# Kernel tuning notes

Hardware: AMD Instinct MI355X
Metric: run time of the kernel (lower is better)

## Reference

```python
import jax, jax.numpy as jnp
import numpy as np

POOL = 2

def conv1x1(x, w, b):
    # x: [B,C,H,W], w: [O,C], b: [O]
    return jnp.einsum('bchw,oc->bohw', x, w) + b[None, :, None, None]

def setup_inputs() -> dict:
    key = jax.random.key(0)
    ks = jax.random.split(key, 8)
    B, C, H, W = 4, 256, 128, 128
    C8 = C // 8
    x = jax.random.normal(ks[0], (B, C, H, W), dtype=jnp.float32)
    wq = jax.random.normal(ks[1], (C8, C), dtype=jnp.float32) * 0.05
    bq = jax.random.normal(ks[2], (C8,), dtype=jnp.float32) * 0.01
    wk = jax.random.normal(ks[3], (C8, C), dtype=jnp.float32) * 0.05
    bk = jax.random.normal(ks[4], (C8,), dtype=jnp.float32) * 0.01
    wv = jax.random.normal(ks[5], (C, C), dtype=jnp.float32) * 0.05
    bv = jax.random.normal(ks[6], (C,), dtype=jnp.float32) * 0.01
    gamma = jnp.full((1,), 0.5, dtype=jnp.float32)  # module inits to 0; nonzero for a meaningful baseline
    return {"x": x, "wq": wq, "bq": bq, "wk": wk, "bk": bk, "wv": wv, "bv": bv, "gamma": gamma}

def reference(x, wq, bq, wk, bk, wv, bv, gamma):
    B, C, H, W = x.shape
    y = x
    # AvgPool2d(pool_size=2)
    Hp, Wp = H // POOL, W // POOL
    xp = x.reshape(B, C, Hp, POOL, Wp, POOL).mean(axis=(3, 5))
    N = Hp * Wp
    q = conv1x1(xp, wq, bq).reshape(B, -1, N)            # [B, C/8, N]
    k = conv1x1(xp, wk, bk).reshape(B, -1, N)            # [B, C/8, N]
    v = conv1x1(xp, wv, bv).reshape(B, C, N)             # [B, C, N]
    energy = jnp.einsum('bcn,bcm->bnm', q, k)            # [B, N, N]
    attn = jax.nn.softmax(energy, axis=-1)
    out = jnp.einsum('bcm,bnm->bcn', v, attn)            # [B, C, N]
    out = out.reshape(B, C, Hp, Wp)
    # bilinear upsample x2, align_corners=False == half-pixel == jax.image.resize 'linear'
    up = jax.image.resize(out, (B, C, H, W), method='bilinear')
    return gamma[0] * up + y
```

## Files before the change

kernel.cpp:

```cpp
#include <hip/hip_runtime.h>

#define BB 4
#define CC 256
#define HH 128
#define WW 128
#define HP 64
#define NP 4096

#define L2E 1.4426950408889634f

typedef __attribute__((ext_vector_type(4)))  float f32x4;
typedef __attribute__((ext_vector_type(16))) float f32x16;
typedef __attribute__((ext_vector_type(8)))  short bf16x8;
typedef __attribute__((ext_vector_type(4)))  unsigned int u32x4;
typedef __attribute__((ext_vector_type(2)))  unsigned int u32x2;
typedef __attribute__((ext_vector_type(2)))  __bf16 bf16x2_t;

static __device__ __forceinline__ float exp2fast(float x) {
    return __builtin_amdgcn_exp2f(x);
}

static __device__ __forceinline__ unsigned short f2bf(float f) {
    unsigned int u = __float_as_uint(f);
    u = (u + 0x7FFFu + ((u >> 16) & 1u)) >> 16;
    return (unsigned short)u;
}
static __device__ __forceinline__ unsigned int pk2(float a, float b) {
    bf16x2_t v = {(__bf16)a, (__bf16)b};
    return __builtin_bit_cast(unsigned int, v);
}
static __device__ __forceinline__ u32x2 plswap(unsigned int a, unsigned int b) {
    return __builtin_amdgcn_permlane32_swap(a, b, false, false);
}


__global__ __launch_bounds__(256) void prep_kernel(const float* __restrict__ x,
                                                   const float* __restrict__ wq,
                                                   const float* __restrict__ wk,
                                                   const float* __restrict__ wv,
                                                   unsigned short* __restrict__ xfrag,
                                                   unsigned short* __restrict__ wfrag) {
    if (blockIdx.x < 2048) {
        int tid  = blockIdx.x * 256 + threadIdx.x;
        int lane = tid & 63;
        int ks   = (tid >> 6) & 15;
        int nt   = (tid >> 10) & 127;
        int b    = tid >> 17;

        int n  = nt * 32 + (lane & 31);
        int c0 = ks * 16 + (lane >> 5) * 8;
        int hp = n >> 6, wp = n & 63;

        const float* xb = x + (size_t)b * CC * (HH * WW) + (2 * hp) * WW + 2 * wp;
        unsigned short r[8];
        #pragma unroll
        for (int e = 0; e < 8; e++) {
            const float* src = xb + (size_t)(c0 + e) * (HH * WW);
            float2 a = *(const float2*)(src);
            float2 d = *(const float2*)(src + WW);
            r[e] = f2bf(0.25f * (a.x + a.y + d.x + d.y));
        }
        ushort4 lo = (ushort4){r[0], r[1], r[2], r[3]};
        ushort4 hi = (ushort4){r[4], r[5], r[6], r[7]};
        *(ushort4*)(xfrag + (size_t)tid * 8)     = lo;
        *(ushort4*)(xfrag + (size_t)tid * 8 + 4) = hi;
    } else {
        int tid  = (blockIdx.x - 2048) * 256 + threadIdx.x;
        if (tid >= 10240) return;
        int lane = tid & 63;
        int ks   = (tid >> 6) & 15;
        int ot   = tid >> 10;

        int o = ot * 32 + (lane & 31);
        int c = ks * 16 + (lane >> 5) * 8;
        const float* wrow;
        float scale = 1.0f;
        if (o < 32)      { wrow = wq + (size_t)o * CC;        scale = L2E; }
        else if (o < 64) { wrow = wk + (size_t)(o - 32) * CC; }
        else             { wrow = wv + (size_t)(o - 64) * CC; }
        float4 w0 = *(const float4*)(wrow + c);
        float4 w1 = *(const float4*)(wrow + c + 4);
        ushort4 lo = {f2bf(w0.x * scale), f2bf(w0.y * scale), f2bf(w0.z * scale), f2bf(w0.w * scale)};
        ushort4 hi = {f2bf(w1.x * scale), f2bf(w1.y * scale), f2bf(w1.z * scale), f2bf(w1.w * scale)};
        *(ushort4*)(wfrag + (size_t)tid * 8)     = lo;
        *(ushort4*)(wfrag + (size_t)tid * 8 + 4) = hi;
    }
}

__global__ __launch_bounds__(128) void projm_kernel(const unsigned short* __restrict__ xfrag,
                                                    const unsigned short* __restrict__ wfrag,
                                                    const float* __restrict__ bq,
                                                    const float* __restrict__ bk,
                                                    const float* __restrict__ bv,
                                                    unsigned short* __restrict__ qarr,
                                                    unsigned short* __restrict__ karr,
                                                    unsigned short* __restrict__ varr) {
    int j    = blockIdx.x;
    int og   = j % 5;
    int nt   = (j / 5) & 127;
    int b    = j / 640;
    int lane = threadIdx.x & 63;
    int ot   = og * 2 + (threadIdx.x >> 6);

    const unsigned short* abase = wfrag + ((size_t)ot * 16 * 64 + lane) * 8;
    const unsigned short* bbase = xfrag + (((size_t)(b * 128 + nt) * 16) * 64 + lane) * 8;

    f32x16 acc;
    #pragma unroll
    for (int r = 0; r < 16; r++) acc[r] = 0.f;

    #pragma unroll
    for (int ks = 0; ks < 16; ks++) {
        bf16x8 af = *(const bf16x8*)(abase + (size_t)ks * 512);
        bf16x8 bf = *(const bf16x8*)(bbase + (size_t)ks * 512);
        acc = __builtin_amdgcn_mfma_f32_32x32x16_bf16(af, bf, acc, 0, 0, 0);
    }

    int l31 = lane & 31;
    int hi2 = lane >> 5;

    if (ot == 0) {
        unsigned short* qb = qarr + (size_t)b * (NP * 32);
        #pragma unroll
        for (int r = 0; r < 16; r++) {
            int o = (r & 3) + 8 * (r >> 2) + 4 * hi2;
            float v = acc[r] + bq[o] * L2E;
            size_t idx = (((size_t)nt * 2 + (o >> 4)) * 32 + l31) * 16 + ((o >> 3) & 1) * 8 + (o & 7);
            qb[idx] = f2bf(v);
        }
    } else if (ot == 1) {
        unsigned short* kb = karr + (size_t)b * (NP * 32);
        #pragma unroll
        for (int r = 0; r < 16; r++) {
            int o = (r & 3) + 8 * (r >> 2) + 4 * hi2;
            float v = acc[r] + bk[o];
            size_t idx = (((size_t)nt * 2 + (o >> 4)) * 32 + l31) * 16 + ((o >> 3) & 1) * 8 + (o & 7);
            kb[idx] = f2bf(v);
        }
    } else {
        unsigned short* vb = varr + (size_t)b * (CC * NP);
        int kc = nt, w2 = (l31 >> 4) & 1, hiv = (l31 >> 3) & 1, ev = l31 & 7;
        size_t base = (((size_t)kc * 2 + w2) * 8) * 32 * 16 + hiv * 8 + ev;
        #pragma unroll
        for (int r = 0; r < 16; r++) {
            int c = (ot - 2) * 32 + (r & 3) + 8 * (r >> 2) + 4 * hi2;
            float v = acc[r] + bv[c];
            size_t idx = base + ((size_t)(c >> 5) * 32 + (c & 31)) * 16;
            vb[idx] = f2bf(v);
        }
    }
}

__global__ __launch_bounds__(256, 2) void flash32_kernel(const unsigned short* __restrict__ qarr,
                                                         const unsigned short* __restrict__ karr,
                                                         const unsigned short* __restrict__ varr,
                                                         float* __restrict__ att) {
    __shared__ float cacc[64][140];
    __shared__ float cml[64][2];
    int t    = threadIdx.x;
    int lane = t & 63;
    int ks   = t >> 6;
    int j    = blockIdx.x;
    int b    = j & 3;
    int qt   = j >> 2;

    const unsigned short* qb2 = qarr + (size_t)b * (NP * 32);
    const unsigned short* kb2 = karr + (size_t)b * (NP * 32);
    const unsigned short* vb2 = varr + (size_t)b * (CC * NP);

    int q  = lane & 31;
    int hi = lane >> 5;
    int lq16 = (q * 2 + hi) * 8;

    bf16x8 qf0 = *(const bf16x8*)(qb2 + (size_t)(qt * 2 + 0) * 512 + lq16);
    bf16x8 qf1 = *(const bf16x8*)(qb2 + (size_t)(qt * 2 + 1) * 512 + lq16);

    f32x16 acc[8];
    #pragma unroll
    for (int ct = 0; ct < 8; ct++)
        #pragma unroll
        for (int r = 0; r < 16; r++) acc[ct][r] = 0.f;
    float mrun = -3.0e38f, lrun = 0.f;

    const f32x16 z16 = {0.f,0.f,0.f,0.f,0.f,0.f,0.f,0.f,0.f,0.f,0.f,0.f,0.f,0.f,0.f,0.f};

    int kc0 = ks * 32;
    const unsigned short* kcp0 = kb2 + (size_t)kc0 * 1024 + lq16;
    bf16x8 kcur0 = *(const bf16x8*)(kcp0);
    bf16x8 kcur1 = *(const bf16x8*)(kcp0 + 512);
    bf16x8 vfA[8], vfB[8];
    {
        const unsigned short* vcp0 = vb2 + ((size_t)kc0 * 16) * 512 + lq16;
        #pragma unroll
        for (int i = 0; i < 8; i++) vfA[i] = *(const bf16x8*)(vcp0 + (size_t)i * 512);
        #pragma unroll
        for (int i = 0; i < 8; i++) vfB[i] = *(const bf16x8*)(vcp0 + (size_t)(8 + i) * 512);
    }

    for (int kci = 0; kci < 32; ++kci) {
        int kcidx = kc0 + kci;
        int nid = (kci < 31) ? (kcidx + 1) : kcidx;

        const unsigned short* kn = kb2 + (size_t)nid * 1024 + lq16;
        bf16x8 kn0 = *(const bf16x8*)(kn);
        bf16x8 kn1 = *(const bf16x8*)(kn + 512);

        f32x16 s = __builtin_amdgcn_mfma_f32_32x32x16_bf16(kcur0, qf0, z16, 0, 0, 0);
        s = __builtin_amdgcn_mfma_f32_32x32x16_bf16(kcur1, qf1, s, 0, 0, 0);

        float m01 = fmaxf(s[0], s[1]),   m23 = fmaxf(s[2], s[3]);
        float m45 = fmaxf(s[4], s[5]),   m67 = fmaxf(s[6], s[7]);
        float m89 = fmaxf(s[8], s[9]),   mab = fmaxf(s[10], s[11]);
        float mcd = fmaxf(s[12], s[13]), mef = fmaxf(s[14], s[15]);
        float mx = fmaxf(fmaxf(fmaxf(m01, m23), fmaxf(m45, m67)),
                         fmaxf(fmaxf(m89, mab), fmaxf(mcd, mef)));
        {
            u32x2 mr = plswap(__float_as_uint(mx), __float_as_uint(mx));
            mx = fmaxf(__uint_as_float(mr.x), __uint_as_float(mr.y));
        }

        if (!__all(mx - mrun <= 11.5f)) {
            float mn = fmaxf(mrun, mx);
            float sc = exp2fast(mrun - mn);
            mrun = mn;
            lrun *= sc;
            #pragma unroll
            for (int ct = 0; ct < 8; ct++)
                #pragma unroll
                for (int r = 0; r < 16; r++) acc[ct][r] *= sc;
        }

        unsigned int pkr[8];
        float ps[8];
        #pragma unroll
        for (int r2 = 0; r2 < 8; r2++) {
            float p0 = exp2fast(s[2 * r2]     - mrun);
            float p1 = exp2fast(s[2 * r2 + 1] - mrun);
            ps[r2] = p0 + p1;
            pkr[r2] = pk2(p0, p1);
        }
        float s01 = ps[0] + ps[1], s23 = ps[2] + ps[3];
        float s45 = ps[4] + ps[5], s67 = ps[6] + ps[7];
        float ss = (s01 + s23) + (s45 + s67);
        {
            u32x2 sr = plswap(__float_as_uint(ss), __float_as_uint(ss));
            ss = __uint_as_float(sr.x) + __uint_as_float(sr.y);
        }
        lrun += ss;

        const unsigned short* vnp = vb2 + ((size_t)nid * 16) * 512 + lq16;

        {
            u32x2 r0 = plswap(pkr[0], pkr[2]);
            u32x2 r1 = plswap(pkr[1], pkr[3]);
            u32x4 fr; fr[0] = r0.x; fr[1] = r1.x; fr[2] = r0.y; fr[3] = r1.y;
            bf16x8 pf = __builtin_bit_cast(bf16x8, fr);
            #pragma unroll
            for (int ct = 0; ct < 8; ct++)
                acc[ct] = __builtin_amdgcn_mfma_f32_32x32x16_bf16(vfA[ct], pf, acc[ct], 0, 0, 0);
            #pragma unroll
            for (int i = 0; i < 8; i++)
                vfA[i] = *(const bf16x8*)(vnp + (size_t)i * 512);
        }

        {
            u32x2 r0 = plswap(pkr[4], pkr[6]);
            u32x2 r1 = plswap(pkr[5], pkr[7]);
            u32x4 fr; fr[0] = r0.x; fr[1] = r1.x; fr[2] = r0.y; fr[3] = r1.y;
            bf16x8 pf = __builtin_bit_cast(bf16x8, fr);
            #pragma unroll
            for (int ct = 0; ct < 8; ct++)
                acc[ct] = __builtin_amdgcn_mfma_f32_32x32x16_bf16(vfB[ct], pf, acc[ct], 0, 0, 0);
            #pragma unroll
            for (int i = 0; i < 8; i++)
                vfB[i] = *(const bf16x8*)(vnp + (size_t)(8 + i) * 512);
        }

        kcur0 = kn0; kcur1 = kn1;
    }

    for (int sIdx = 3; sIdx >= 1; --sIdx) {
        if (ks == sIdx) {
            #pragma unroll
            for (int ct = 0; ct < 8; ct++)
                #pragma unroll
                for (int rr = 0; rr < 4; rr++) {
                    float4 v4 = {acc[ct][rr*4+0], acc[ct][rr*4+1], acc[ct][rr*4+2], acc[ct][rr*4+3]};
                    *(float4*)&cacc[lane][ct * 16 + rr * 4] = v4;
                }
            cml[lane][0] = mrun; cml[lane][1] = lrun;
        }
        __syncthreads();
        if (ks == 0) {
            float mo = cml[lane][0];
            float lo = cml[lane][1];
            float mn = fmaxf(mrun, mo);
            float e0 = exp2fast(mrun - mn);
            float e1 = exp2fast(mo - mn);
            mrun = mn;
            lrun = lrun * e0 + lo * e1;
            #pragma unroll
            for (int ct = 0; ct < 8; ct++)
                #pragma unroll
                for (int r = 0; r < 16; r++)
                    acc[ct][r] = acc[ct][r] * e0 + cacc[lane][ct * 16 + r] * e1;
        }
        __syncthreads();
    }

    if (ks == 0) {
        float inv = 1.0f / lrun;
        #pragma unroll
        for (int ct = 0; ct < 8; ct++)
            #pragma unroll
            for (int r = 0; r < 16; r++) {
                int c = ct * 32 + (r & 3) + 8 * (r >> 2) + 4 * hi;
                att[((size_t)b * CC + c) * NP + qt * 32 + q] = acc[ct][r] * inv;
            }
    }
}

__global__ __launch_bounds__(256) void upsample_kernel(const float* __restrict__ att,
                                                       const float* __restrict__ x,
                                                       const float* __restrict__ gamma,
                                                       float* __restrict__ out) {
    int tid = blockIdx.x * 256 + threadIdx.x;
    int w4 = (tid & 31) * 4;
    int h  = (tid >> 5) & 127;
    int bc = tid >> 12;
    float g = gamma[0];

    float sh = 0.5f * h - 0.25f;
    float fhf = floorf(sh);
    float th = sh - fhf;
    int ih = (int)fhf;
    int ih0 = ih < 0 ? 0 : ih;
    int ih1 = ih + 1 > 63 ? 63 : ih + 1;
    const float* a0r = att + (size_t)bc * NP + ih0 * 64;
    const float* a1r = att + (size_t)bc * NP + ih1 * 64;

    float4 xin = *(const float4*)(x + (size_t)bc * (HH * WW) + h * WW + w4);
    float xv[4] = {xin.x, xin.y, xin.z, xin.w};
    float ov[4];
    #pragma unroll
    for (int k = 0; k < 4; k++) {
        int w = w4 + k;
        float sw = 0.5f * w - 0.25f;
        float fwf = floorf(sw);
        float tw = sw - fwf;
        int iw = (int)fwf;
        int iw0 = iw < 0 ? 0 : iw;
        int iw1 = iw + 1 > 63 ? 63 : iw + 1;
        float v00 = a0r[iw0], v01 = a0r[iw1];
        float v10 = a1r[iw0], v11 = a1r[iw1];
        float top = v00 + tw * (v01 - v00);
        float bot = v10 + tw * (v11 - v10);
        float up  = top + th * (bot - top);
        ov[k] = g * up + xv[k];
    }
    float4 o4 = {ov[0], ov[1], ov[2], ov[3]};
    *(float4*)(out + (size_t)bc * (HH * WW) + h * WW + w4) = o4;
}

extern "C" void kernel_launch(void* const* d_in, const int* in_sizes, int n_in,
                              void* d_out, int out_size, void* d_ws, size_t ws_size,
                              hipStream_t stream) {
    (void)in_sizes; (void)n_in; (void)out_size; (void)ws_size;
    const float* x     = (const float*)d_in[0];
    const float* wq    = (const float*)d_in[1];
    const float* bq    = (const float*)d_in[2];
    const float* wk    = (const float*)d_in[3];
    const float* bk    = (const float*)d_in[4];
    const float* wv    = (const float*)d_in[5];
    const float* bv    = (const float*)d_in[6];
    const float* gamma = (const float*)d_in[7];
    float* out = (float*)d_out;

    unsigned short* xfrag = (unsigned short*)d_ws;
    unsigned short* wfrag = xfrag + 4194304;
    unsigned short* qarr  = wfrag + 131072;
    unsigned short* karr  = qarr + 524288;
    unsigned short* varr  = karr + 524288;
    float*          att   = (float*)(varr + 4194304);

    prep_kernel<<<2088, 256, 0, stream>>>(x, wq, wk, wv, xfrag, wfrag);
    projm_kernel<<<2560, 128, 0, stream>>>(xfrag, wfrag, bq, bk, bv, qarr, karr, varr);
    flash32_kernel<<<512, 256, 0, stream>>>(qarr, karr, varr, att);
    upsample_kernel<<<16384, 256, 0, stream>>>(att, x, gamma, out);
}
```

Measured before the change: 120.1 us.

## Process two query tiles per block and split value channels across wave pairs

```diff
diff --git a/kernel.cpp b/kernel.cpp
--- a/kernel.cpp
+++ b/kernel.cpp
@@ -151,18 +151,21 @@
     }
 }
 
-__global__ __launch_bounds__(256, 2) void flash32_kernel(const unsigned short* __restrict__ qarr,
+__global__ __launch_bounds__(512, 2) void flash32_kernel(const unsigned short* __restrict__ qarr,
                                                          const unsigned short* __restrict__ karr,
                                                          const unsigned short* __restrict__ varr,
                                                          float* __restrict__ att) {
-    __shared__ float cacc[64][140];
-    __shared__ float cml[64][2];
+    __shared__ float cacc[2][64][68];
+    __shared__ float cml[2][64][2];
     int t    = threadIdx.x;
     int lane = t & 63;
-    int ks   = t >> 6;
+    int w    = t >> 6;
+    int ch   = w & 1;
+    int ks   = w >> 1;
     int j    = blockIdx.x;
     int b    = j & 3;
-    int qt   = j >> 2;
+    int st   = j >> 2;
+    int qt0  = st * 2, qt1 = qt0 + 1;
 
     const unsigned short* qb2 = qarr + (size_t)b * (NP * 32);
     const unsigned short* kb2 = karr + (size_t)b * (NP * 32);
@@ -172,15 +175,18 @@
     int hi = lane >> 5;
     int lq16 = (q * 2 + hi) * 8;
 
-    bf16x8 qf0 = *(const bf16x8*)(qb2 + (size_t)(qt * 2 + 0) * 512 + lq16);
-    bf16x8 qf1 = *(const bf16x8*)(qb2 + (size_t)(qt * 2 + 1) * 512 + lq16);
-
-    f32x16 acc[8];
+    bf16x8 qA0 = *(const bf16x8*)(qb2 + (size_t)(qt0 * 2 + 0) * 512 + lq16);
+    bf16x8 qA1 = *(const bf16x8*)(qb2 + (size_t)(qt0 * 2 + 1) * 512 + lq16);
+    bf16x8 qB0 = *(const bf16x8*)(qb2 + (size_t)(qt1 * 2 + 0) * 512 + lq16);
+    bf16x8 qB1 = *(const bf16x8*)(qb2 + (size_t)(qt1 * 2 + 1) * 512 + lq16);
+
+    f32x16 accA[4], accB[4];
     #pragma unroll
-    for (int ct = 0; ct < 8; ct++)
-        #pragma unroll
-        for (int r = 0; r < 16; r++) acc[ct][r] = 0.f;
-    float mrun = -3.0e38f, lrun = 0.f;
+    for (int ct = 0; ct < 4; ct++)
+        #pragma unroll
+        for (int r = 0; r < 16; r++) { accA[ct][r] = 0.f; accB[ct][r] = 0.f; }
+    float mrunA = -3.0e38f, lrunA = 0.f;
+    float mrunB = -3.0e38f, lrunB = 0.f;
 
     const f32x16 z16 = {0.f,0.f,0.f,0.f,0.f,0.f,0.f,0.f,0.f,0.f,0.f,0.f,0.f,0.f,0.f,0.f};
 
@@ -188,134 +194,171 @@
     const unsigned short* kcp0 = kb2 + (size_t)kc0 * 1024 + lq16;
     bf16x8 kcur0 = *(const bf16x8*)(kcp0);
     bf16x8 kcur1 = *(const bf16x8*)(kcp0 + 512);
-    bf16x8 vfA[8], vfB[8];
-    {
-        const unsigned short* vcp0 = vb2 + ((size_t)kc0 * 16) * 512 + lq16;
-        #pragma unroll
-        for (int i = 0; i < 8; i++) vfA[i] = *(const bf16x8*)(vcp0 + (size_t)i * 512);
-        #pragma unroll
-        for (int i = 0; i < 8; i++) vfB[i] = *(const bf16x8*)(vcp0 + (size_t)(8 + i) * 512);
-    }
 
     for (int kci = 0; kci < 32; ++kci) {
         int kcidx = kc0 + kci;
         int nid = (kci < 31) ? (kcidx + 1) : kcidx;
 
+        const unsigned short* vcp = vb2 + ((size_t)kcidx * 16 + ch * 4) * 512 + lq16;
+        bf16x8 vf[8];
+        #pragma unroll
+        for (int w2 = 0; w2 < 2; w2++)
+            #pragma unroll
+            for (int i = 0; i < 4; i++)
+                vf[w2 * 4 + i] = *(const bf16x8*)(vcp + (size_t)(w2 * 8 + i) * 512);
+
         const unsigned short* kn = kb2 + (size_t)nid * 1024 + lq16;
         bf16x8 kn0 = *(const bf16x8*)(kn);
         bf16x8 kn1 = *(const bf16x8*)(kn + 512);
 
-        f32x16 s = __builtin_amdgcn_mfma_f32_32x32x16_bf16(kcur0, qf0, z16, 0, 0, 0);
-        s = __builtin_amdgcn_mfma_f32_32x32x16_bf16(kcur1, qf1, s, 0, 0, 0);
-
-        float m01 = fmaxf(s[0], s[1]),   m23 = fmaxf(s[2], s[3]);
-        float m45 = fmaxf(s[4], s[5]),   m67 = fmaxf(s[6], s[7]);
-        float m89 = fmaxf(s[8], s[9]),   mab = fmaxf(s[10], s[11]);
-        float mcd = fmaxf(s[12], s[13]), mef = fmaxf(s[14], s[15]);
-        float mx = fmaxf(fmaxf(fmaxf(m01, m23), fmaxf(m45, m67)),
-                         fmaxf(fmaxf(m89, mab), fmaxf(mcd, mef)));
+        f32x16 sA = __builtin_amdgcn_mfma_f32_32x32x16_bf16(kcur0, qA0, z16, 0, 0, 0);
+        sA = __builtin_amdgcn_mfma_f32_32x32x16_bf16(kcur1, qA1, sA, 0, 0, 0);
+        f32x16 sB = __builtin_amdgcn_mfma_f32_32x32x16_bf16(kcur0, qB0, z16, 0, 0, 0);
+        sB = __builtin_amdgcn_mfma_f32_32x32x16_bf16(kcur1, qB1, sB, 0, 0, 0);
+
+        unsigned int pkrA[8];
         {
+            float m01 = fmaxf(sA[0], sA[1]),   m23 = fmaxf(sA[2], sA[3]);
+            float m45 = fmaxf(sA[4], sA[5]),   m67 = fmaxf(sA[6], sA[7]);
+            float m89 = fmaxf(sA[8], sA[9]),   mab = fmaxf(sA[10], sA[11]);
+            float mcd = fmaxf(sA[12], sA[13]), mef = fmaxf(sA[14], sA[15]);
+            float mx = fmaxf(fmaxf(fmaxf(m01, m23), fmaxf(m45, m67)),
+                             fmaxf(fmaxf(m89, mab), fmaxf(mcd, mef)));
             u32x2 mr = plswap(__float_as_uint(mx), __float_as_uint(mx));
             mx = fmaxf(__uint_as_float(mr.x), __uint_as_float(mr.y));
-        }
-
-        if (!__all(mx - mrun <= 11.5f)) {
-            float mn = fmaxf(mrun, mx);
-            float sc = exp2fast(mrun - mn);
-            mrun = mn;
-            lrun *= sc;
+            if (!__all(mx - mrunA <= 11.5f)) {
+                float mn = fmaxf(mrunA, mx);
+                float sc = exp2fast(mrunA - mn);
+                mrunA = mn;
+                lrunA *= sc;
+                #pragma unroll
+                for (int ct = 0; ct < 4; ct++)
+                    #pragma unroll
+                    for (int r = 0; r < 16; r++) accA[ct][r] *= sc;
+            }
+            float ps[8];
             #pragma unroll
-            for (int ct = 0; ct < 8; ct++)
+            for (int r2 = 0; r2 < 8; r2++) {
+                float p0 = exp2fast(sA[2 * r2]     - mrunA);
+                float p1 = exp2fast(sA[2 * r2 + 1] - mrunA);
+                ps[r2] = p0 + p1;
+                pkrA[r2] = pk2(p0, p1);
+            }
+            float s01 = ps[0] + ps[1], s23 = ps[2] + ps[3];
+            float s45 = ps[4] + ps[5], s67 = ps[6] + ps[7];
+            float ssum = (s01 + s23) + (s45 + s67);
+            u32x2 sr = plswap(__float_as_uint(ssum), __float_as_uint(ssum));
+            lrunA += __uint_as_float(sr.x) + __uint_as_float(sr.y);
+        }
+
+        unsigned int pkrB[8];
+        {
+            float m01 = fmaxf(sB[0], sB[1]),   m23 = fmaxf(sB[2], sB[3]);
+            float m45 = fmaxf(sB[4], sB[5]),   m67 = fmaxf(sB[6], sB[7]);
+            float m89 = fmaxf(sB[8], sB[9]),   mab = fmaxf(sB[10], sB[11]);
+            float mcd = fmaxf(sB[12], sB[13]), mef = fmaxf(sB[14], sB[15]);
+            float mx = fmaxf(fmaxf(fmaxf(m01, m23), fmaxf(m45, m67)),
+                             fmaxf(fmaxf(m89, mab), fmaxf(mcd, mef)));
+            u32x2 mr = plswap(__float_as_uint(mx), __float_as_uint(mx));
+            mx = fmaxf(__uint_as_float(mr.x), __uint_as_float(mr.y));
+            if (!__all(mx - mrunB <= 11.5f)) {
+                float mn = fmaxf(mrunB, mx);
+                float sc = exp2fast(mrunB - mn);
+                mrunB = mn;
+                lrunB *= sc;
                 #pragma unroll
-                for (int r = 0; r < 16; r++) acc[ct][r] *= sc;
-        }
-
-        unsigned int pkr[8];
-        float ps[8];
-        #pragma unroll
-        for (int r2 = 0; r2 < 8; r2++) {
-            float p0 = exp2fast(s[2 * r2]     - mrun);
-            float p1 = exp2fast(s[2 * r2 + 1] - mrun);
-            ps[r2] = p0 + p1;
-            pkr[r2] = pk2(p0, p1);
-        }
-        float s01 = ps[0] + ps[1], s23 = ps[2] + ps[3];
-        float s45 = ps[4] + ps[5], s67 = ps[6] + ps[7];
-        float ss = (s01 + s23) + (s45 + s67);
-        {
-            u32x2 sr = plswap(__float_as_uint(ss), __float_as_uint(ss));
-            ss = __uint_as_float(sr.x) + __uint_as_float(sr.y);
-        }
-        lrun += ss;
-
-        const unsigned short* vnp = vb2 + ((size_t)nid * 16) * 512 + lq16;
-
-        {
-            u32x2 r0 = plswap(pkr[0], pkr[2]);
-            u32x2 r1 = plswap(pkr[1], pkr[3]);
-            u32x4 fr; fr[0] = r0.x; fr[1] = r1.x; fr[2] = r0.y; fr[3] = r1.y;
-            bf16x8 pf = __builtin_bit_cast(bf16x8, fr);
+                for (int ct = 0; ct < 4; ct++)
+                    #pragma unroll
+                    for (int r = 0; r < 16; r++) accB[ct][r] *= sc;
+            }
+            float ps[8];
             #pragma unroll
-            for (int ct = 0; ct < 8; ct++)
-                acc[ct] = __builtin_amdgcn_mfma_f32_32x32x16_bf16(vfA[ct], pf, acc[ct], 0, 0, 0);
+            for (int r2 = 0; r2 < 8; r2++) {
+                float p0 = exp2fast(sB[2 * r2]     - mrunB);
+                float p1 = exp2fast(sB[2 * r2 + 1] - mrunB);
+                ps[r2] = p0 + p1;
+                pkrB[r2] = pk2(p0, p1);
+            }
+            float s01 = ps[0] + ps[1], s23 = ps[2] + ps[3];
+            float s45 = ps[4] + ps[5], s67 = ps[6] + ps[7];
+            float ssum = (s01 + s23) + (s45 + s67);
+            u32x2 sr = plswap(__float_as_uint(ssum), __float_as_uint(ssum));
+            lrunB += __uint_as_float(sr.x) + __uint_as_float(sr.y);
+        }
+
+        #pragma unroll
+        for (int w2 = 0; w2 < 2; w2++) {
+            u32x2 rA0 = plswap(pkrA[4 * w2 + 0], pkrA[4 * w2 + 2]);
+            u32x2 rA1 = plswap(pkrA[4 * w2 + 1], pkrA[4 * w2 + 3]);
+            u32x4 frA; frA[0] = rA0.x; frA[1] = rA1.x; frA[2] = rA0.y; frA[3] = rA1.y;
+            bf16x8 pfA = __builtin_bit_cast(bf16x8, frA);
+            u32x2 rB0 = plswap(pkrB[4 * w2 + 0], pkrB[4 * w2 + 2]);
+            u32x2 rB1 = plswap(pkrB[4 * w2 + 1], pkrB[4 * w2 + 3]);
+            u32x4 frB; frB[0] = rB0.x; frB[1] = rB1.x; frB[2] = rB0.y; frB[3] = rB1.y;
+            bf16x8 pfB = __builtin_bit_cast(bf16x8, frB);
             #pragma unroll
-            for (int i = 0; i < 8; i++)
-                vfA[i] = *(const bf16x8*)(vnp + (size_t)i * 512);
-        }
-
-        {
-            u32x2 r0 = plswap(pkr[4], pkr[6]);
-            u32x2 r1 = plswap(pkr[5], pkr[7]);
-            u32x4 fr; fr[0] = r0.x; fr[1] = r1.x; fr[2] = r0.y; fr[3] = r1.y;
-            bf16x8 pf = __builtin_bit_cast(bf16x8, fr);
-            #pragma unroll
-            for (int ct = 0; ct < 8; ct++)
-                acc[ct] = __builtin_amdgcn_mfma_f32_32x32x16_bf16(vfB[ct], pf, acc[ct], 0, 0, 0);
-            #pragma unroll
-            for (int i = 0; i < 8; i++)
-                vfB[i] = *(const bf16x8*)(vnp + (size_t)(8 + i) * 512);
+            for (int ct = 0; ct < 4; ct++) {
+                accA[ct] = __builtin_amdgcn_mfma_f32_32x32x16_bf16(vf[w2 * 4 + ct], pfA, accA[ct], 0, 0, 0);
+                accB[ct] = __builtin_amdgcn_mfma_f32_32x32x16_bf16(vf[w2 * 4 + ct], pfB, accB[ct], 0, 0, 0);
+            }
         }
 
         kcur0 = kn0; kcur1 = kn1;
     }
 
-    for (int sIdx = 3; sIdx >= 1; --sIdx) {
-        if (ks == sIdx) {
-            #pragma unroll
-            for (int ct = 0; ct < 8; ct++)
+    #pragma unroll
+    for (int tile = 0; tile < 2; tile++) {
+        for (int sIdx = 3; sIdx >= 1; --sIdx) {
+            if (ks == sIdx) {
                 #pragma unroll
-                for (int rr = 0; rr < 4; rr++) {
-                    float4 v4 = {acc[ct][rr*4+0], acc[ct][rr*4+1], acc[ct][rr*4+2], acc[ct][rr*4+3]};
-                    *(float4*)&cacc[lane][ct * 16 + rr * 4] = v4;
-                }
-            cml[lane][0] = mrun; cml[lane][1] = lrun;
-        }
-        __syncthreads();
-        if (ks == 0) {
-            float mo = cml[lane][0];
-            float lo = cml[lane][1];
-            float mn = fmaxf(mrun, mo);
-            float e0 = exp2fast(mrun - mn);
-            float e1 = exp2fast(mo - mn);
-            mrun = mn;
-            lrun = lrun * e0 + lo * e1;
-            #pragma unroll
-            for (int ct = 0; ct < 8; ct++)
+                for (int ct = 0; ct < 4; ct++)
+                    #pragma unroll
+                    for (int rr = 0; rr < 4; rr++) {
+                        float4 v4;
+                        if (tile == 0)
+                            v4 = (float4){accA[ct][rr*4+0], accA[ct][rr*4+1], accA[ct][rr*4+2], accA[ct][rr*4+3]};
+                        else
+                            v4 = (float4){accB[ct][rr*4+0], accB[ct][rr*4+1], accB[ct][rr*4+2], accB[ct][rr*4+3]};
+                        *(float4*)&cacc[ch][lane][ct * 16 + rr * 4] = v4;
+                    }
+                cml[ch][lane][0] = (tile == 0) ? mrunA : mrunB;
+                cml[ch][lane][1] = (tile == 0) ? lrunA : lrunB;
+            }
+            __syncthreads();
+            if (ks == 0) {
+                float mo = cml[ch][lane][0];
+                float lo = cml[ch][lane][1];
+                float mr = (tile == 0) ? mrunA : mrunB;
+                float mn = fmaxf(mr, mo);
+                float e0 = exp2fast(mr - mn);
+                float e1 = exp2fast(mo - mn);
+                if (tile == 0) { mrunA = mn; lrunA = lrunA * e0 + lo * e1; }
+                else           { mrunB = mn; lrunB = lrunB * e0 + lo * e1; }
                 #pragma unroll
-                for (int r = 0; r < 16; r++)
-                    acc[ct][r] = acc[ct][r] * e0 + cacc[lane][ct * 16 + r] * e1;
-        }
-        __syncthreads();
+                for (int ct = 0; ct < 4; ct++)
+                    #pragma unroll
+                    for (int r = 0; r < 16; r++) {
+                        if (tile == 0)
+                            accA[ct][r] = accA[ct][r] * e0 + cacc[ch][lane][ct * 16 + r] * e1;
+                        else
+                            accB[ct][r] = accB[ct][r] * e0 + cacc[ch][lane][ct * 16 + r] * e1;
+                    }
+            }
+            __syncthreads();
+        }
     }
 
     if (ks == 0) {
-        float inv = 1.0f / lrun;
-        #pragma unroll
-        for (int ct = 0; ct < 8; ct++)
+        float invA = 1.0f / lrunA;
+        float invB = 1.0f / lrunB;
+        #pragma unroll
+        for (int ct = 0; ct < 4; ct++)
             #pragma unroll
             for (int r = 0; r < 16; r++) {
-                int c = ct * 32 + (r & 3) + 8 * (r >> 2) + 4 * hi;
-                att[((size_t)b * CC + c) * NP + qt * 32 + q] = acc[ct][r] * inv;
+                int c = ch * 128 + ct * 32 + (r & 3) + 8 * (r >> 2) + 4 * hi;
+                float* ob = att + ((size_t)b * CC + c) * NP;
+                ob[qt0 * 32 + q] = accA[ct][r] * invA;
+                ob[qt1 * 32 + q] = accB[ct][r] * invB;
             }
     }
 }
@@ -385,6 +428,6 @@
 
     prep_kernel<<<2088, 256, 0, stream>>>(x, wq, wk, wv, xfrag, wfrag);
     projm_kernel<<<2560, 128, 0, stream>>>(xfrag, wfrag, bq, bk, bv, qarr, karr, varr);
-    flash32_kernel<<<512, 256, 0, stream>>>(qarr, karr, varr, att);
+    flash32_kernel<<<256, 512, 0, stream>>>(qarr, karr, varr, att);
     upsample_kernel<<<16384, 256, 0, stream>>>(att, x, gamma, out);
 }
```

Measured after the change: 119.2 us. No clear change (-0.8%).
